# Performance work log

Measured on AMD Instinct MI355X. Metric: run time of the kernel, lower is better.

Reference implementation:

```python
import jax, jax.numpy as jnp
import numpy as np

EPS = 1e-8
B, T, D = 2, 512, 64
L = 4        # n_layers
NPASS = 2    # n_recursive_passes


def setup_inputs() -> dict:
    key = jax.random.key(0)
    ks = jax.random.split(key, 8)
    H = D // 2
    r = lambda k, shape, s=0.05: jax.random.normal(k, shape, dtype=jnp.float32) * s
    return {
        "basin_seq": jax.random.normal(ks[0], (B, T, D), dtype=jnp.float32),
        "basin_coords": r(ks[1], (D,), 0.1),
        "W_temp": r(ks[2], (L, 1, D)),
        "b_temp": jnp.zeros((L, 1), jnp.float32),
        "res_scale": jnp.full((L,), 0.1, jnp.float32),
        "W_fb": r(ks[3], (L, D, 2 * D)),
        "b_fb": jnp.zeros((L, D), jnp.float32),
        "Wc1": r(ks[4], (H, D)),
        "bc1": jnp.zeros((H,), jnp.float32),
        "Wc2": r(ks[5], (D, H)),
        "bc2": jnp.zeros((D,), jnp.float32),
        "Wu": r(ks[6], (D, 2 * D)),
        "bu": jnp.zeros((D,), jnp.float32),
        "res_scale_g": jnp.asarray(1.0, jnp.float32),
    }


def _project_to_simplex(x):
    s = jax.nn.softplus(x)
    s = s / (s.sum(axis=-1, keepdims=True) + EPS)
    return jnp.maximum(s, EPS)


def _qfi_attention_weights(x, temperature):
    # x: (B,T,D); temperature: scalar
    p = _project_to_simplex(x)
    # fisher_rao_distance_simplex renormalizes its inputs again
    p = p / (p.sum(axis=-1, keepdims=True) + EPS)
    # pairwise Bhattacharyya-like inner product: (B,T,T,D) broadcast -> (B,T,T)
    inner = jnp.sqrt(p[:, :, None, :] * p[:, None, :, :] + EPS).sum(axis=-1)
    inner = jnp.clip(inner, -1.0 + 1e-6, 1.0 - 1e-6)
    d = 2.0 * jnp.arccos(inner)                      # Fisher-Rao distance (B,T,T)
    logits = -d / jnp.maximum(temperature, 1e-6)
    return jax.nn.softmax(logits, axis=-1)


def _forward(basin_seq, basin_coords, W_temp, b_temp, res_scale, W_fb, b_fb,
             Wc1, bc1, Wc2, bc2, Wu, bu, res_scale_g):
    x = basin_seq
    current_basin = basin_coords                     # (D,)
    layer_states = [[None] * L for _ in range(NPASS)]
    for p_idx in range(NPASS):
        for l in range(L):
            prev = layer_states[p_idx - 1][l] if p_idx > 0 else None
            if prev is not None:
                combined = jnp.concatenate([x, prev], axis=-1)          # (B,T,2D)
                gate = jax.nn.sigmoid(combined @ W_fb[l].T + b_fb[l])   # (B,T,D)
                x = x * gate + prev * (1.0 - gate)
            # BasinCoupledQFIAttention (dropout inactive in eval)
            tm = jax.nn.sigmoid(W_temp[l] @ current_basin + b_temp[l]) + 0.5
            temperature = jax.lax.stop_gradient(tm.mean())  # torch uses .item()
            w = _qfi_attention_weights(x, temperature)
            x_attn = jnp.einsum('bij,bjd->bid', w, x)
            x = x + res_scale[l] * (x_attn - x)
            layer_states[p_idx][l] = x
        # holographic encode: mean-pool then compress MLP (tanh, tanh)
        pooled = x.mean(axis=1)                                         # (B,D)
        hidden_basin = jnp.tanh(jnp.tanh(pooled @ Wc1.T + bc1) @ Wc2.T + bc2)
        if p_idx < NPASS - 1:
            aggregated = hidden_basin.mean(axis=0)                      # (D,)
            comb = jnp.concatenate([current_basin, aggregated], axis=-1)
            g = jax.nn.sigmoid(Wu @ comb + bu)
            current_basin = current_basin * (1.0 - g) + aggregated * g
    output = x + 0.01 * res_scale_g * (x - basin_seq)
    return output


def reference(basin_seq, basin_coords, W_temp, b_temp, res_scale, W_fb, b_fb,
              Wc1, bc1, Wc2, bc2, Wu, bu, res_scale_g):
    return _forward(basin_seq, basin_coords, W_temp, b_temp, res_scale, W_fb,
                    b_fb, Wc1, bc1, Wc2, bc2, Wu, bu, res_scale_g)
```

## Files before the change

kernel.cpp:

```cpp
#include <hip/hip_runtime.h>
#include <math.h>

#define EPSF 1e-8f
#define Tn 512
#define Dn 64
#define ROWS 1024
#define NELEM 65536

typedef _Float16 half_t;
typedef __attribute__((ext_vector_type(4))) _Float16 half4;

__device__ __forceinline__ float sigmoidf_(float x){ return 1.0f/(1.0f+expf(-x)); }
__device__ __forceinline__ float softplusf_(float x){ return fmaxf(x,0.0f) + log1pf(expf(-fabsf(x))); }

__device__ __forceinline__ float wrs(float v){
  #pragma unroll
  for (int off=1; off<64; off<<=1) v += __shfl_xor(v, off, 64);
  return v;
}
__device__ __forceinline__ float wrm(float v){
  #pragma unroll
  for (int off=1; off<64; off<<=1) v = fmaxf(v, __shfl_xor(v, off, 64));
  return v;
}

__device__ __forceinline__ void pnorm_w(float xg, int b, int r, int row, int d,
                                        float* __restrict__ sbuf_out,
                                        half_t* __restrict__ sTh_out){
  float s = softplusf_(xg);
  float sum = wrs(s);
  float p = fmaxf(s/(sum+EPSF), EPSF);
  float s2 = wrs(p);
  float sq = sqrtf(p/(s2+EPSF));
  sbuf_out[(size_t)row*Dn + d] = sq;
  sTh_out[(size_t)b*Dn*Tn + (size_t)d*Tn + r] = (half_t)sq;
}

__global__ __launch_bounds__(256) void k_prologue(
    const float* __restrict__ basin_seq, float* __restrict__ sA, half_t* __restrict__ sThA,
    half_t* __restrict__ xhBS,
    const float* __restrict__ W_temp, const float* __restrict__ b_temp,
    const float* __restrict__ cb0, float* __restrict__ temps){
  int tid = threadIdx.x, wid = tid>>6, lane = tid&63;
  if (blockIdx.x < 256){
    int row = blockIdx.x*4 + wid;
    float xv = basin_seq[(size_t)row*Dn+lane];
    xhBS[(size_t)row*Dn+lane] = (half_t)xv;
    pnorm_w(xv, row>>9, row&511, row, lane, sA, sThA);
  } else if (tid < 64){
    float cbv = cb0[tid];
    #pragma unroll
    for (int l=0;l<4;l++){
      float v = wrs(W_temp[l*Dn + tid]*cbv);
      if (tid==0) temps[l] = sigmoidf_(v + b_temp[l]) + 0.5f;
    }
  }
}

__device__ __forceinline__ void gate_dot2(float (*comb)[128], float* gred,
                                          const float* __restrict__ Wfb, int tid, int lane){
  int dd = tid >> 3, k8 = tid & 7;
  const float4* wp = (const float4*)(Wfb + (size_t)dd*128 + k8*16);
  float4 w0 = wp[0], w1 = wp[1], w2 = wp[2], w3 = wp[3];
  float ga[2];
  #pragma unroll
  for (int i=0;i<2;i++){
    float4 c0 = *(const float4*)&comb[i][k8*16];
    float4 c1 = *(const float4*)&comb[i][k8*16+4];
    float4 c2 = *(const float4*)&comb[i][k8*16+8];
    float4 c3 = *(const float4*)&comb[i][k8*16+12];
    ga[i] = w0.x*c0.x + w0.y*c0.y + w0.z*c0.z + w0.w*c0.w
          + w1.x*c1.x + w1.y*c1.y + w1.z*c1.z + w1.w*c1.w
          + w2.x*c2.x + w2.y*c2.y + w2.z*c2.z + w2.w*c2.w
          + w3.x*c3.x + w3.y*c3.y + w3.z*c3.z + w3.w*c3.w;
  }
  #pragma unroll
  for (int off=1; off<8; off<<=1){
    ga[0] += __shfl_xor(ga[0],off,64); ga[1] += __shfl_xor(ga[1],off,64);
  }
  if ((lane&7)==0){ gred[dd*3+0]=ga[0]; gred[dd*3+1]=ga[1]; }
}

template<int MODE>
__global__ __launch_bounds__(512) void k_attn(
    const float* __restrict__ xin, const half_t* __restrict__ xh,
    const float* __restrict__ sbuf, const half_t* __restrict__ sTh,
    const float* __restrict__ temps, const float* __restrict__ res_scale, int l,
    float* __restrict__ xout, half_t* __restrict__ xh_out,
    float* __restrict__ sbuf_out, half_t* __restrict__ sTh_out,
    const float* __restrict__ Wfb, const float* __restrict__ bfb,
    const float* __restrict__ prev,
    const float* __restrict__ basin_seq, const float* __restrict__ rsg){
  __shared__ __align__(16) union {
    float part[8*512];
    float pvp[32*2*64];
  } u;
  __shared__ __align__(8) float P[512*2];
  __shared__ __align__(8) float s_i[64*2];
  __shared__ float redw[2][8][2];
  __shared__ __align__(16) float comb[2][128];
  __shared__ float gred[64*3];

  int tid = threadIdx.x, wav = tid>>6, lane = tid&63;
  int row0 = blockIdx.x*2, b = row0>>9, r0 = row0&511;
  int i_ = tid>>6, d_ = lane;

  float xi_pre = 0.f, prev_pre = 0.f;
  if (tid < 128){
    s_i[d_*2 + i_] = sbuf[(size_t)(row0+i_)*Dn + d_];
    xi_pre = xin[(size_t)(row0+i_)*Dn + d_];
    if constexpr (MODE == 2) prev_pre = prev[(size_t)(row0+i_)*Dn + d_];
  }
  __syncthreads();

  float invT = 1.0f/fmaxf(temps[l], 1e-6f);
  {
    int g = tid & 127, kq = tid >> 7;
    const half4* sT4 = (const half4*)(sTh + (size_t)b*Dn*Tn);
    float4 a0 = {0,0,0,0}, a1 = a0;
    int kb = kq*16;
    #pragma unroll
    for (int kk=0; kk<16; ++kk){
      int k = kb + kk;
      half4 vh = sT4[(size_t)k*128 + g];
      float vx=(float)vh.x, vy=(float)vh.y, vz=(float)vh.z, vw=(float)vh.w;
      float2 si = *(const float2*)&s_i[k*2];
      a0.x=fmaf(si.x,vx,a0.x); a0.y=fmaf(si.x,vy,a0.y);
      a0.z=fmaf(si.x,vz,a0.z); a0.w=fmaf(si.x,vw,a0.w);
      a1.x=fmaf(si.y,vx,a1.x); a1.y=fmaf(si.y,vy,a1.y);
      a1.z=fmaf(si.y,vz,a1.z); a1.w=fmaf(si.y,vw,a1.w);
    }
    *(float4*)&u.part[(0*4+kq)*512 + g*4] = a0;
    *(float4*)&u.part[(1*4+kq)*512 + g*4] = a1;
  }
  __syncthreads();
  {
    int j = tid;
    float a0 = u.part[0*512+j] + u.part[1*512+j] + u.part[2*512+j] + u.part[3*512+j];
    float a1 = u.part[4*512+j] + u.part[5*512+j] + u.part[6*512+j] + u.part[7*512+j];
    float l0 = -2.0f*acosf(fminf(fmaxf(a0,-1.0f+1e-6f),1.0f-1e-6f))*invT;
    float l1 = -2.0f*acosf(fminf(fmaxf(a1,-1.0f+1e-6f),1.0f-1e-6f))*invT;
    float m0=wrm(l0), m1=wrm(l1);
    if (lane==0){ redw[0][wav][0]=m0; redw[0][wav][1]=m1; }
    __syncthreads();
    float mv0=redw[0][0][0], mv1=redw[0][0][1];
    #pragma unroll
    for (int w=1;w<8;w++){ mv0=fmaxf(mv0,redw[0][w][0]); mv1=fmaxf(mv1,redw[0][w][1]); }
    float e0=expf(l0-mv0), e1=expf(l1-mv1);
    float2 ev = {e0,e1};
    *(float2*)&P[j*2] = ev;
    float q0=wrs(e0), q1=wrs(e1);
    if (lane==0){ redw[1][wav][0]=q0; redw[1][wav][1]=q1; }
  }
  __syncthreads();
  {
    int jg = tid>>4, dq = tid&15;
    const half4* x4 = (const half4*)(xh + (size_t)b*Tn*Dn);
    float4 o0={0,0,0,0}, o1=o0;
    int jb = jg*16;
    #pragma unroll
    for (int jj=0; jj<16; ++jj){
      int j = jb + jj;
      half4 xvh = x4[(size_t)j*16 + dq];
      float xx=(float)xvh.x, xy=(float)xvh.y, xz=(float)xvh.z, xw=(float)xvh.w;
      float2 pw = *(const float2*)&P[j*2];
      o0.x=fmaf(pw.x,xx,o0.x); o0.y=fmaf(pw.x,xy,o0.y);
      o0.z=fmaf(pw.x,xz,o0.z); o0.w=fmaf(pw.x,xw,o0.w);
      o1.x=fmaf(pw.y,xx,o1.x); o1.y=fmaf(pw.y,xy,o1.y);
      o1.z=fmaf(pw.y,xz,o1.z); o1.w=fmaf(pw.y,xw,o1.w);
    }
    *(float4*)&u.pvp[(jg*2+0)*64 + dq*4] = o0;
    *(float4*)&u.pvp[(jg*2+1)*64 + dq*4] = o1;
  }
  __syncthreads();
  float o = 0.f;
  if (tid < 128){
    float ss = 0.f;
    #pragma unroll
    for (int jg=0; jg<32; ++jg) ss += u.pvp[(jg*2+i_)*64+d_];
    float sv = 0.f;
    #pragma unroll
    for (int w=0;w<8;w++) sv += redw[1][w][i_];
    float attn = ss/sv;
    o = xi_pre + res_scale[l]*(attn - xi_pre);
  }
  if constexpr (MODE == 0){
    if (tid < 128){
      xout[(size_t)(row0+i_)*Dn + d_] = o;
      xh_out[(size_t)(row0+i_)*Dn + d_] = (half_t)o;
      pnorm_w(o, b, r0+i_, row0+i_, d_, sbuf_out, sTh_out);
    }
  } else if constexpr (MODE == 1){
    if (tid < 128) xout[(size_t)(row0+i_)*Dn + d_] = o;
  } else if constexpr (MODE == 2){
    if (tid < 128){
      comb[i_][d_] = o;
      comb[i_][64+d_] = prev_pre;
    }
    __syncthreads();
    gate_dot2(comb, gred, Wfb, tid, lane);
    __syncthreads();
    if (tid < 128){
      float g = sigmoidf_(gred[d_*3+i_] + bfb[d_]);
      float xg = o*g + prev_pre*(1.0f-g);
      xout[(size_t)(row0+i_)*Dn + d_] = xg;
      xh_out[(size_t)(row0+i_)*Dn + d_] = (half_t)xg;
      pnorm_w(xg, b, r0+i_, row0+i_, d_, sbuf_out, sTh_out);
    }
  } else {
    if (tid < 128){
      float c = 0.01f * rsg[0];
      xout[(size_t)(row0+i_)*Dn + d_] = o + c*(o - basin_seq[(size_t)(row0+i_)*Dn + d_]);
    }
  }
}

__global__ __launch_bounds__(256) void k_basinprep(
    const float* __restrict__ st3, const float* __restrict__ st0,
    const float* __restrict__ W_fb, const float* __restrict__ b_fb,
    float* __restrict__ xA, half_t* __restrict__ xhA,
    float* __restrict__ sA, half_t* __restrict__ sThA,
    const float* __restrict__ Wc1, const float* __restrict__ bc1,
    const float* __restrict__ Wc2, const float* __restrict__ bc2,
    const float* __restrict__ Wu,  const float* __restrict__ bu,
    const float* __restrict__ cb_in, float* __restrict__ cb_out,
    const float* __restrict__ W_temp, const float* __restrict__ b_temp,
    float* __restrict__ temps){
  int tid = threadIdx.x, wid = tid>>6, lane = tid&63;
  __shared__ __align__(16) float comb4[4][128];
  __shared__ float pooled[128];
  __shared__ float h1[64];
  __shared__ float hb[128];
  __shared__ float combb[128];
  if (blockIdx.x < 256){
    int row = blockIdx.x*4 + wid;
    float xv = st3[(size_t)row*Dn+lane];
    float pvv = st0[(size_t)row*Dn+lane];
    comb4[wid][lane] = xv; comb4[wid][64+lane] = pvv;
    __syncthreads();
    const float4* W  = (const float4*)(W_fb + (size_t)lane*128);
    const float4* c4 = (const float4*)comb4[wid];
    float g0=0.f,g1=0.f;
    #pragma unroll
    for (int k=0;k<32;k+=2){
      float4 w0=W[k],   c0=c4[k];
      float4 w1=W[k+1], c1=c4[k+1];
      g0 += w0.x*c0.x + w0.y*c0.y + w0.z*c0.z + w0.w*c0.w;
      g1 += w1.x*c1.x + w1.y*c1.y + w1.z*c1.z + w1.w*c1.w;
    }
    float g = sigmoidf_(g0+g1 + b_fb[lane]);
    float xg = xv*g + pvv*(1.0f-g);
    xA[(size_t)row*Dn+lane] = xg;
    xhA[(size_t)row*Dn+lane] = (half_t)xg;
    pnorm_w(xg, row>>9, row&511, row, lane, sA, sThA);
  } else {
    if (tid < 128){
      int b = tid >> 6, d = tid & 63;
      float acc=0.f;
      const float* xb = st3 + (size_t)b*Tn*Dn + d;
      for (int t=0;t<Tn;t++) acc += xb[(size_t)t*Dn];
      pooled[tid] = acc * (1.0f/Tn);
    }
    __syncthreads();
    if (tid < 64){
      int b = tid >> 5, h = tid & 31;
      float acc=0.f;
      #pragma unroll 8
      for (int d2=0; d2<64; d2++) acc += pooled[b*64+d2]*Wc1[h*64+d2];
      h1[tid] = tanhf(acc + bc1[h]);
    }
    __syncthreads();
    if (tid < 128){
      int b = tid >> 6, d = tid & 63;
      float acc=0.f;
      #pragma unroll 8
      for (int h2=0; h2<32; h2++) acc += h1[b*32+h2]*Wc2[d*32+h2];
      hb[tid] = tanhf(acc + bc2[d]);
    }
    __syncthreads();
    if (tid < 64){
      float agg = 0.5f*(hb[tid] + hb[64+tid]);
      combb[tid] = cb_in[tid];
      combb[64+tid] = agg;
    }
    __syncthreads();
    if (tid < 64){
      float acc=0.f;
      #pragma unroll 8
      for (int k=0;k<128;k++) acc += Wu[tid*128+k]*combb[k];
      float g = sigmoidf_(acc + bu[tid]);
      float nb = combb[tid]*(1.0f-g) + combb[64+tid]*g;
      cb_out[tid] = nb;
      #pragma unroll
      for (int l=0;l<4;l++){
        float v = wrs(W_temp[l*Dn + tid]*nb);
        if (tid==0) temps[l] = sigmoidf_(v + b_temp[l]) + 0.5f;
      }
    }
  }
}

extern "C" void kernel_launch(void* const* d_in, const int* in_sizes, int n_in,
                              void* d_out, int out_size, void* d_ws, size_t ws_size,
                              hipStream_t stream) {
  const float* basin_seq    = (const float*)d_in[0];
  const float* basin_coords = (const float*)d_in[1];
  const float* W_temp       = (const float*)d_in[2];
  const float* b_temp       = (const float*)d_in[3];
  const float* res_scale    = (const float*)d_in[4];
  const float* W_fb         = (const float*)d_in[5];
  const float* b_fb         = (const float*)d_in[6];
  const float* Wc1          = (const float*)d_in[7];
  const float* bc1          = (const float*)d_in[8];
  const float* Wc2          = (const float*)d_in[9];
  const float* bc2          = (const float*)d_in[10];
  const float* Wu           = (const float*)d_in[11];
  const float* bu           = (const float*)d_in[12];
  const float* rsg          = (const float*)d_in[13];
  float* out = (float*)d_out;
  float* ws  = (float*)d_ws;

  const size_t N = NELEM;
  float* sA    = ws;
  float* sB    = ws + N;
  float* st    = ws + 2*N;
  float* xA    = ws + 6*N;
  float* xB    = ws + 7*N;
  half_t* sThA = (half_t*)(ws + 8*N);
  half_t* sThB = (half_t*)(ws + 8*N + N/2);
  half_t* xhBS = (half_t*)(ws + 9*N);
  half_t* xhA  = (half_t*)(ws + 9*N + N/2);
  half_t* xhB  = (half_t*)(ws + 10*N);
  float* temps = ws + 10*N + N/2;
  float* cb    = ws + 10*N + N/2 + 64;
  float* st0 = st, *st1 = st+N, *st2 = st+2*N, *st3 = st+3*N;

  const int GA = 512;

  k_prologue<<<257,256,0,stream>>>(basin_seq, sA, sThA, xhBS, W_temp, b_temp, basin_coords, temps);
  k_attn<0><<<GA,512,0,stream>>>(basin_seq, xhBS, sA, sThA, temps, res_scale, 0,
                                 st0, xhA, sB, sThB, nullptr,nullptr,nullptr,nullptr,nullptr);
  k_attn<0><<<GA,512,0,stream>>>(st0, xhA, sB, sThB, temps, res_scale, 1,
                                 st1, xhB, sA, sThA, nullptr,nullptr,nullptr,nullptr,nullptr);
  k_attn<0><<<GA,512,0,stream>>>(st1, xhB, sA, sThA, temps, res_scale, 2,
                                 st2, xhA, sB, sThB, nullptr,nullptr,nullptr,nullptr,nullptr);
  k_attn<1><<<GA,512,0,stream>>>(st2, xhA, sB, sThB, temps, res_scale, 3,
                                 st3, nullptr, nullptr, nullptr, nullptr,nullptr,nullptr,nullptr,nullptr);
  k_basinprep<<<257,256,0,stream>>>(st3, st0, W_fb, b_fb, xA, xhA, sA, sThA,
                                    Wc1, bc1, Wc2, bc2, Wu, bu,
                                    basin_coords, cb, W_temp, b_temp, temps);
  k_attn<2><<<GA,512,0,stream>>>(xA, xhA, sA, sThA, temps, res_scale, 0,
                                 xB, xhB, sB, sThB,
                                 W_fb + (size_t)1*Dn*2*Dn, b_fb + 1*Dn, st1, nullptr,nullptr);
  k_attn<2><<<GA,512,0,stream>>>(xB, xhB, sB, sThB, temps, res_scale, 1,
                                 xA, xhA, sA, sThA,
                                 W_fb + (size_t)2*Dn*2*Dn, b_fb + 2*Dn, st2, nullptr,nullptr);
  k_attn<2><<<GA,512,0,stream>>>(xA, xhA, sA, sThA, temps, res_scale, 2,
                                 xB, xhB, sB, sThB,
                                 W_fb + (size_t)3*Dn*2*Dn, b_fb + 3*Dn, st3, nullptr,nullptr);
  k_attn<3><<<GA,512,0,stream>>>(xB, xhB, sB, sThB, temps, res_scale, 3,
                                 out, nullptr, nullptr, nullptr,
                                 nullptr,nullptr,nullptr, basin_seq, rsg);
}
```

Measured before the change: 176.0 us.

## Fuse basin update and first gate into last-layer attention, drop basinprep kernel

Removes the separate k_basinprep kernel. The last first-pass attention layer now computes the layer-0 feedback gate itself and accumulates mean-pool sums with atomics. Each second-pass attention block recomputes the small compress/update MLP and its layer temperature redundantly from the pooled sums. This saves one launch and the serial pooling block, but adds a memset, global atomics, and per-block redundant MLP work, and the atomic summation order is nondeterministic.

```diff
diff --git a/kernel.cpp b/kernel.cpp
--- a/kernel.cpp
+++ b/kernel.cpp
@@ -4,7 +4,6 @@
 #define EPSF 1e-8f
 #define Tn 512
 #define Dn 64
-#define ROWS 1024
 #define NELEM 65536
 
 typedef _Float16 half_t;
@@ -86,11 +85,16 @@
     const float* __restrict__ xin, const half_t* __restrict__ xh,
     const float* __restrict__ sbuf, const half_t* __restrict__ sTh,
     const float* __restrict__ temps, const float* __restrict__ res_scale, int l,
-    float* __restrict__ xout, half_t* __restrict__ xh_out,
+    float* __restrict__ xout, float* __restrict__ xg_out, half_t* __restrict__ xh_out,
     float* __restrict__ sbuf_out, half_t* __restrict__ sTh_out,
     const float* __restrict__ Wfb, const float* __restrict__ bfb,
     const float* __restrict__ prev,
-    const float* __restrict__ basin_seq, const float* __restrict__ rsg){
+    const float* __restrict__ basin_seq, const float* __restrict__ rsg,
+    float* __restrict__ pooled_g, const float* __restrict__ basin_coords,
+    const float* __restrict__ Wc1, const float* __restrict__ bc1,
+    const float* __restrict__ Wc2, const float* __restrict__ bc2,
+    const float* __restrict__ Wu,  const float* __restrict__ bu,
+    const float* __restrict__ W_temp, const float* __restrict__ b_temp){
   __shared__ __align__(16) union {
     float part[8*512];
     float pvp[32*2*64];
@@ -100,6 +104,8 @@
   __shared__ float redw[2][8][2];
   __shared__ __align__(16) float comb[2][128];
   __shared__ float gred[64*3];
+  __shared__ float pl[128], h1b[64], hbb[128], combb[128];
+  __shared__ float tl_sh;
 
   int tid = threadIdx.x, wav = tid>>6, lane = tid&63;
   int row0 = blockIdx.x*2, b = row0>>9, r0 = row0&511;
@@ -109,11 +115,46 @@
   if (tid < 128){
     s_i[d_*2 + i_] = sbuf[(size_t)(row0+i_)*Dn + d_];
     xi_pre = xin[(size_t)(row0+i_)*Dn + d_];
-    if constexpr (MODE == 2) prev_pre = prev[(size_t)(row0+i_)*Dn + d_];
+    if constexpr (MODE == 4 || MODE == 5) prev_pre = prev[(size_t)(row0+i_)*Dn + d_];
+  }
+
+  if constexpr (MODE == 5 || MODE == 6){
+    if (tid < 128) pl[tid] = pooled_g[tid] * (1.0f/512.0f);
+    __syncthreads();
+    if (tid < 64){
+      int bb=tid>>5, h=tid&31;
+      float acc=0.f;
+      #pragma unroll 8
+      for (int d2=0; d2<64; d2++) acc += pl[bb*64+d2]*Wc1[h*64+d2];
+      h1b[tid] = tanhf(acc + bc1[h]);
+    }
+    __syncthreads();
+    if (tid < 128){
+      int bb=tid>>6, dd=tid&63;
+      float acc=0.f;
+      #pragma unroll 8
+      for (int h2=0; h2<32; h2++) acc += h1b[bb*32+h2]*Wc2[dd*32+h2];
+      hbb[tid] = tanhf(acc + bc2[dd]);
+    }
+    __syncthreads();
+    if (tid < 64){
+      float agg = 0.5f*(hbb[tid] + hbb[64+tid]);
+      combb[tid] = basin_coords[tid];
+      combb[64+tid] = agg;
+    }
+    __syncthreads();
+    if (tid < 64){
+      float acc=0.f;
+      #pragma unroll 8
+      for (int k=0;k<128;k++) acc += Wu[tid*128+k]*combb[k];
+      float g = sigmoidf_(acc + bu[tid]);
+      float cbl = combb[tid]*(1.0f-g) + combb[64+tid]*g;
+      float v = wrs(W_temp[l*Dn + tid]*cbl);
+      if (tid==0) tl_sh = sigmoidf_(v + b_temp[l]) + 0.5f;
+    }
   }
   __syncthreads();
 
-  float invT = 1.0f/fmaxf(temps[l], 1e-6f);
   {
     int g = tid & 127, kq = tid >> 7;
     const half4* sT4 = (const half4*)(sTh + (size_t)b*Dn*Tn);
@@ -135,6 +176,9 @@
   }
   __syncthreads();
   {
+    float invT;
+    if constexpr (MODE == 5 || MODE == 6) invT = 1.0f/fmaxf(tl_sh, 1e-6f);
+    else invT = 1.0f/fmaxf(temps[l], 1e-6f);
     int j = tid;
     float a0 = u.part[0*512+j] + u.part[1*512+j] + u.part[2*512+j] + u.part[3*512+j];
     float a1 = u.part[4*512+j] + u.part[5*512+j] + u.part[6*512+j] + u.part[7*512+j];
@@ -190,9 +234,24 @@
       xh_out[(size_t)(row0+i_)*Dn + d_] = (half_t)o;
       pnorm_w(o, b, r0+i_, row0+i_, d_, sbuf_out, sTh_out);
     }
-  } else if constexpr (MODE == 1){
-    if (tid < 128) xout[(size_t)(row0+i_)*Dn + d_] = o;
-  } else if constexpr (MODE == 2){
+  } else if constexpr (MODE == 4){
+    if (tid < 128){
+      xout[(size_t)(row0+i_)*Dn + d_] = o;
+      atomicAdd(&pooled_g[b*64+d_], o);
+      comb[i_][d_] = o;
+      comb[i_][64+d_] = prev_pre;
+    }
+    __syncthreads();
+    gate_dot2(comb, gred, Wfb, tid, lane);
+    __syncthreads();
+    if (tid < 128){
+      float g = sigmoidf_(gred[d_*3+i_] + bfb[d_]);
+      float xg = o*g + prev_pre*(1.0f-g);
+      xg_out[(size_t)(row0+i_)*Dn + d_] = xg;
+      xh_out[(size_t)(row0+i_)*Dn + d_] = (half_t)xg;
+      pnorm_w(xg, b, r0+i_, row0+i_, d_, sbuf_out, sTh_out);
+    }
+  } else if constexpr (MODE == 5){
     if (tid < 128){
       comb[i_][d_] = o;
       comb[i_][64+d_] = prev_pre;
@@ -211,91 +270,6 @@
     if (tid < 128){
       float c = 0.01f * rsg[0];
       xout[(size_t)(row0+i_)*Dn + d_] = o + c*(o - basin_seq[(size_t)(row0+i_)*Dn + d_]);
-    }
-  }
-}
-
-__global__ __launch_bounds__(256) void k_basinprep(
-    const float* __restrict__ st3, const float* __restrict__ st0,
-    const float* __restrict__ W_fb, const float* __restrict__ b_fb,
-    float* __restrict__ xA, half_t* __restrict__ xhA,
-    float* __restrict__ sA, half_t* __restrict__ sThA,
-    const float* __restrict__ Wc1, const float* __restrict__ bc1,
-    const float* __restrict__ Wc2, const float* __restrict__ bc2,
-    const float* __restrict__ Wu,  const float* __restrict__ bu,
-    const float* __restrict__ cb_in, float* __restrict__ cb_out,
-    const float* __restrict__ W_temp, const float* __restrict__ b_temp,
-    float* __restrict__ temps){
-  int tid = threadIdx.x, wid = tid>>6, lane = tid&63;
-  __shared__ __align__(16) float comb4[4][128];
-  __shared__ float pooled[128];
-  __shared__ float h1[64];
-  __shared__ float hb[128];
-  __shared__ float combb[128];
-  if (blockIdx.x < 256){
-    int row = blockIdx.x*4 + wid;
-    float xv = st3[(size_t)row*Dn+lane];
-    float pvv = st0[(size_t)row*Dn+lane];
-    comb4[wid][lane] = xv; comb4[wid][64+lane] = pvv;
-    __syncthreads();
-    const float4* W  = (const float4*)(W_fb + (size_t)lane*128);
-    const float4* c4 = (const float4*)comb4[wid];
-    float g0=0.f,g1=0.f;
-    #pragma unroll
-    for (int k=0;k<32;k+=2){
-      float4 w0=W[k],   c0=c4[k];
-      float4 w1=W[k+1], c1=c4[k+1];
-      g0 += w0.x*c0.x + w0.y*c0.y + w0.z*c0.z + w0.w*c0.w;
-      g1 += w1.x*c1.x + w1.y*c1.y + w1.z*c1.z + w1.w*c1.w;
-    }
-    float g = sigmoidf_(g0+g1 + b_fb[lane]);
-    float xg = xv*g + pvv*(1.0f-g);
-    xA[(size_t)row*Dn+lane] = xg;
-    xhA[(size_t)row*Dn+lane] = (half_t)xg;
-    pnorm_w(xg, row>>9, row&511, row, lane, sA, sThA);
-  } else {
-    if (tid < 128){
-      int b = tid >> 6, d = tid & 63;
-      float acc=0.f;
-      const float* xb = st3 + (size_t)b*Tn*Dn + d;
-      for (int t=0;t<Tn;t++) acc += xb[(size_t)t*Dn];
-      pooled[tid] = acc * (1.0f/Tn);
-    }
-    __syncthreads();
-    if (tid < 64){
-      int b = tid >> 5, h = tid & 31;
-      float acc=0.f;
-      #pragma unroll 8
-      for (int d2=0; d2<64; d2++) acc += pooled[b*64+d2]*Wc1[h*64+d2];
-      h1[tid] = tanhf(acc + bc1[h]);
-    }
-    __syncthreads();
-    if (tid < 128){
-      int b = tid >> 6, d = tid & 63;
-      float acc=0.f;
-      #pragma unroll 8
-      for (int h2=0; h2<32; h2++) acc += h1[b*32+h2]*Wc2[d*32+h2];
-      hb[tid] = tanhf(acc + bc2[d]);
-    }
-    __syncthreads();
-    if (tid < 64){
-      float agg = 0.5f*(hb[tid] + hb[64+tid]);
-      combb[tid] = cb_in[tid];
-      combb[64+tid] = agg;
-    }
-    __syncthreads();
-    if (tid < 64){
-      float acc=0.f;
-      #pragma unroll 8
-      for (int k=0;k<128;k++) acc += Wu[tid*128+k]*combb[k];
-      float g = sigmoidf_(acc + bu[tid]);
-      float nb = combb[tid]*(1.0f-g) + combb[64+tid]*g;
-      cb_out[tid] = nb;
-      #pragma unroll
-      for (int l=0;l<4;l++){
-        float v = wrs(W_temp[l*Dn + tid]*nb);
-        if (tid==0) temps[l] = sigmoidf_(v + b_temp[l]) + 0.5f;
-      }
     }
   }
 }
@@ -321,44 +295,58 @@
   float* ws  = (float*)d_ws;
 
   const size_t N = NELEM;
-  float* sA    = ws;
-  float* sB    = ws + N;
-  float* st    = ws + 2*N;
-  float* xA    = ws + 6*N;
-  float* xB    = ws + 7*N;
-  half_t* sThA = (half_t*)(ws + 8*N);
-  half_t* sThB = (half_t*)(ws + 8*N + N/2);
-  half_t* xhBS = (half_t*)(ws + 9*N);
-  half_t* xhA  = (half_t*)(ws + 9*N + N/2);
-  half_t* xhB  = (half_t*)(ws + 10*N);
-  float* temps = ws + 10*N + N/2;
-  float* cb    = ws + 10*N + N/2 + 64;
-  float* st0 = st, *st1 = st+N, *st2 = st+2*N, *st3 = st+3*N;
+  float* pooled_g = ws;
+  float* temps    = ws + 192;
+  float* base     = ws + 256;
+  float* sA    = base;
+  float* sB    = base + N;
+  float* st0   = base + 2*N;
+  float* st1   = base + 3*N;
+  float* st2   = base + 4*N;
+  float* st3   = base + 5*N;
+  float* xA    = base + 6*N;
+  float* xB    = base + 7*N;
+  half_t* sThA = (half_t*)(base + 8*N);
+  half_t* sThB = (half_t*)(base + 8*N + N/2);
+  half_t* xhBS = (half_t*)(base + 9*N);
+  half_t* xhA  = (half_t*)(base + 9*N + N/2);
+  half_t* xhB  = (half_t*)(base + 10*N);
 
   const int GA = 512;
+
+  (void)hipMemsetAsync(d_ws, 0, 1024, stream);
 
   k_prologue<<<257,256,0,stream>>>(basin_seq, sA, sThA, xhBS, W_temp, b_temp, basin_coords, temps);
   k_attn<0><<<GA,512,0,stream>>>(basin_seq, xhBS, sA, sThA, temps, res_scale, 0,
-                                 st0, xhA, sB, sThB, nullptr,nullptr,nullptr,nullptr,nullptr);
+                                 st0, nullptr, xhA, sB, sThB,
+                                 nullptr,nullptr,nullptr,nullptr,nullptr,
+                                 nullptr,nullptr,nullptr,nullptr,nullptr,nullptr,nullptr,nullptr,nullptr,nullptr);
   k_attn<0><<<GA,512,0,stream>>>(st0, xhA, sB, sThB, temps, res_scale, 1,
-                                 st1, xhB, sA, sThA, nullptr,nullptr,nullptr,nullptr,nullptr);
+                                 st1, nullptr, xhB, sA, sThA,
+                                 nullptr,nullptr,nullptr,nullptr,nullptr,
+                                 nullptr,nullptr,nullptr,nullptr,nullptr,nullptr,nullptr,nullptr,nullptr,nullptr);
   k_attn<0><<<GA,512,0,stream>>>(st1, xhB, sA, sThA, temps, res_scale, 2,
-                                 st2, xhA, sB, sThB, nullptr,nullptr,nullptr,nullptr,nullptr);
-  k_attn<1><<<GA,512,0,stream>>>(st2, xhA, sB, sThB, temps, res_scale, 3,
-                                 st3, nullptr, nullptr, nullptr, nullptr,nullptr,nullptr,nullptr,nullptr);
-  k_basinprep<<<257,256,0,stream>>>(st3, st0, W_fb, b_fb, xA, xhA, sA, sThA,
-                                    Wc1, bc1, Wc2, bc2, Wu, bu,
-                                    basin_coords, cb, W_temp, b_temp, temps);
-  k_attn<2><<<GA,512,0,stream>>>(xA, xhA, sA, sThA, temps, res_scale, 0,
-                                 xB, xhB, sB, sThB,
-                                 W_fb + (size_t)1*Dn*2*Dn, b_fb + 1*Dn, st1, nullptr,nullptr);
-  k_attn<2><<<GA,512,0,stream>>>(xB, xhB, sB, sThB, temps, res_scale, 1,
-                                 xA, xhA, sA, sThA,
-                                 W_fb + (size_t)2*Dn*2*Dn, b_fb + 2*Dn, st2, nullptr,nullptr);
-  k_attn<2><<<GA,512,0,stream>>>(xA, xhA, sA, sThA, temps, res_scale, 2,
-                                 xB, xhB, sB, sThB,
-                                 W_fb + (size_t)3*Dn*2*Dn, b_fb + 3*Dn, st3, nullptr,nullptr);
-  k_attn<3><<<GA,512,0,stream>>>(xB, xhB, sB, sThB, temps, res_scale, 3,
-                                 out, nullptr, nullptr, nullptr,
-                                 nullptr,nullptr,nullptr, basin_seq, rsg);
-}
+                                 st2, nullptr, xhA, sB, sThB,
+                                 nullptr,nullptr,nullptr,nullptr,nullptr,
+                                 nullptr,nullptr,nullptr,nullptr,nullptr,nullptr,nullptr,nullptr,nullptr,nullptr);
+  k_attn<4><<<GA,512,0,stream>>>(st2, xhA, sB, sThB, temps, res_scale, 3,
+                                 st3, xA, xhBS, sA, sThA,
+                                 W_fb, b_fb, st0, nullptr,nullptr,
+                                 pooled_g,nullptr,nullptr,nullptr,nullptr,nullptr,nullptr,nullptr,nullptr,nullptr);
+  k_attn<5><<<GA,512,0,stream>>>(xA, xhBS, sA, sThA, nullptr, res_scale, 0,
+                                 xB, nullptr, xhA, sB, sThB,
+                                 W_fb + (size_t)1*Dn*2*Dn, b_fb + 1*Dn, st1, nullptr,nullptr,
+                                 pooled_g, basin_coords, Wc1, bc1, Wc2, bc2, Wu, bu, W_temp, b_temp);
+  k_attn<5><<<GA,512,0,stream>>>(xB, xhA, sB, sThB, nullptr, res_scale, 1,
+                                 xA, nullptr, xhB, sA, sThA,
+                                 W_fb + (size_t)2*Dn*2*Dn, b_fb + 2*Dn, st2, nullptr,nullptr,
+                                 pooled_g, basin_coords, Wc1, bc1, Wc2, bc2, Wu, bu, W_temp, b_temp);
+  k_attn<5><<<GA,512,0,stream>>>(xA, xhB, sA, sThA, nullptr, res_scale, 2,
+                                 xB, nullptr, xhA, sB, sThB,
+                                 W_fb + (size_t)3*Dn*2*Dn, b_fb + 3*Dn, st3, nullptr,nullptr,
+                                 pooled_g, basin_coords, Wc1, bc1, Wc2, bc2, Wu, bu, W_temp, b_temp);
+  k_attn<6><<<GA,512,0,stream>>>(xB, xhA, sB, sThB, nullptr, res_scale, 3,
+                                 out, nullptr, nullptr, nullptr, nullptr,
+                                 nullptr,nullptr,nullptr, basin_seq, rsg,
+                                 pooled_g, basin_coords, Wc1, bc1, Wc2, bc2, Wu, bu, W_temp, b_temp);
+}
```

Result: slower. 199.1 us (+13.1%).
